# Kernel tuning notes

Measured on AMD Instinct MI355X. Metric: run time of the kernel, lower is better.

The kernel has to match this reference:

```python
import jax, jax.numpy as jnp
import numpy as np


def setup_inputs() -> dict:
    key = jax.random.key(0)
    k1, k2, k3 = jax.random.split(key, 3)
    B, DIM, H, Wd = 32, 512, 64, 64
    K, DQ = 64, 3
    features = jax.random.normal(k1, (B, DIM, H, Wd), dtype=jnp.float32)
    query = jax.random.normal(k2, (B, DQ, H, Wd), dtype=jnp.float32)
    # Ensemble of K 1x1 convs (no bias): weight [K, dim_query, dim], scaled like conv init
    W = jax.random.normal(k3, (K, DQ, DIM), dtype=jnp.float32) * (1.0 / np.sqrt(DIM))
    return {"features": features, "query": query, "W": W}


def reference(features, query, W):
    B = query.shape[0]
    # ensemble 1x1 conv: key_values [k, b, q, h, w]
    kv = jnp.einsum('kqd,bdhw->kbqhw', W, features)
    # rearrange 'k b ... -> b k ...'
    kv_b = jnp.transpose(kv, (1, 0, 2, 3, 4))          # [b, k, q, h, w]
    q_flat = query.reshape(B, 1, -1)                    # [b, 1, N]
    kv_flat = kv_b.reshape(B, kv_b.shape[1], -1)        # [b, k, N]
    # torch.cdist (p=2) between [b,1,N] and [b,k,N] -> [b,k]
    diff = q_flat - kv_flat
    distance = jnp.sqrt(jnp.sum(diff * diff, axis=-1))  # [b, k]
    codes = jnp.argmin(distance, axis=-1)               # [b]
    # batched gather of selected key_values
    idx = codes[:, None, None, None, None]
    sel_key_values = jnp.take_along_axis(kv_b, idx, axis=1)[:, 0]  # [b, q, h, w]
    commit_loss = jnp.mean((sel_key_values - query) ** 2)
    return sel_key_values, codes, commit_loss
```

## Files before the change

kernel.cpp:

```cpp
#include <hip/hip_runtime.h>
#include <hip/hip_bf16.h>
#include <hip/hip_fp16.h>

#define BN   32
#define DIMK 512
#define HW   4096
#define KK   64
#define DQ   3
#define RR   192
#define NT   128
#define NBLK (HW / NT)

typedef _Float16 half8  __attribute__((ext_vector_type(8)));
typedef float    f32x4  __attribute__((ext_vector_type(4)));
typedef short    short8 __attribute__((ext_vector_type(8)));

#define A16_OFF    0
#define A16_BYTES  (RR * DIMK * 2)
#define DIST2_OFF  196608
#define DIST2_BYTES (BN * KK * 4)
#define KV_OFF     262144
#define KV_BYTES   ((size_t)BN * RR * HW * 2)

#define OUT_SEL    ((size_t)BN * DQ * HW)
#define OUT_LOSS   (OUT_SEL + BN)

__global__ void init_kernel(const float* __restrict__ Wsrc,
                            _Float16* __restrict__ A16,
                            float* __restrict__ dist2,
                            float* __restrict__ out) {
  int gid = blockIdx.x * 256 + threadIdx.x;
  if (gid < RR * DIMK) A16[gid] = (_Float16)Wsrc[gid];
  if (gid < BN * KK)   dist2[gid] = 0.f;
  if (gid == 0)        out[OUT_LOSS] = 0.f;
}

template <bool STORE>
__global__ __launch_bounds__(256) void gemm_dist_kernel(
    const float* __restrict__ f, const float* __restrict__ query,
    const _Float16* __restrict__ A16, __hip_bfloat16* __restrict__ kv,
    float* __restrict__ dist2) {
  __shared__ __align__(16) _Float16 Alds[2][RR][40];
  __shared__ __align__(16) _Float16 Blds[2][4][NT][8];
  __shared__ float qlds[DQ][NT];
  __shared__ float rowsum[RR];

  const int t  = threadIdx.x;
  const int w  = t >> 6;
  const int l  = t & 63;
  const int lq = l >> 4;
  const int ln = l & 15;
  const int b  = blockIdx.y;
  const int n0 = blockIdx.x * NT;

  for (int s = t; s < DQ * NT; s += 256) {
    int q = s / NT, n = s % NT;
    qlds[q][n] = query[((size_t)b * DQ + q) * HW + n0 + n];
  }

  f32x4 acc[3][8];
#pragma unroll
  for (int mt = 0; mt < 3; mt++)
#pragma unroll
    for (int nt = 0; nt < 8; nt++) acc[mt][nt] = (f32x4)0.f;

  const int bn  = t & (NT - 1);
  const int bkb = t >> 7;

  float bpre[16];
  half8 apre[3];

  auto loadTile = [&](int kk) {
    const float* fp = f + ((size_t)b * DIMK + kk * 32 + bkb * 16) * HW + n0 + bn;
#pragma unroll
    for (int j = 0; j < 16; j++) bpre[j] = fp[(size_t)j * HW];
#pragma unroll
    for (int i = 0; i < 3; i++) {
      int s = t + i * 256;
      int m = s >> 2, oct = s & 3;
      apre[i] = *(const half8*)&A16[m * DIMK + kk * 32 + oct * 8];
    }
  };
  auto stageTile = [&](int buf) {
#pragma unroll
    for (int i = 0; i < 3; i++) {
      int s = t + i * 256;
      int m = s >> 2, oct = s & 3;
      *(half8*)&Alds[buf][m][oct * 8] = apre[i];
    }
    half8 h0, h1;
#pragma unroll
    for (int j = 0; j < 8; j++) { h0[j] = (_Float16)bpre[j]; h1[j] = (_Float16)bpre[8 + j]; }
    *(half8*)&Blds[buf][2 * bkb][bn][0]     = h0;
    *(half8*)&Blds[buf][2 * bkb + 1][bn][0] = h1;
  };

  loadTile(0);
  stageTile(0);
  for (int kk = 0; kk < DIMK / 32; kk++) {
    const int cur = kk & 1;
    __syncthreads();
    if (kk < DIMK / 32 - 1) loadTile(kk + 1);

    half8 af[3], bf[8];
#pragma unroll
    for (int mt = 0; mt < 3; mt++)
      af[mt] = *(const half8*)&Alds[cur][w * 48 + mt * 16 + ln][lq * 8];
#pragma unroll
    for (int nt = 0; nt < 8; nt++)
      bf[nt] = *(const half8*)&Blds[cur][lq][nt * 16 + ln][0];
#pragma unroll
    for (int mt = 0; mt < 3; mt++)
#pragma unroll
      for (int nt = 0; nt < 8; nt++)
        acc[mt][nt] = __builtin_amdgcn_mfma_f32_16x16x32_f16(af[mt], bf[nt],
                                                             acc[mt][nt], 0, 0, 0);
    if (kk < DIMK / 32 - 1) stageTile(cur ^ 1);
  }

  float rs[3][4];
#pragma unroll
  for (int mt = 0; mt < 3; mt++)
#pragma unroll
    for (int i = 0; i < 4; i++) rs[mt][i] = 0.f;

#pragma unroll
  for (int mt = 0; mt < 3; mt++) {
#pragma unroll
    for (int i = 0; i < 4; i++) {
      int r = w * 48 + mt * 16 + lq * 4 + i;
      int q = r % 3;
#pragma unroll
      for (int nt = 0; nt < 8; nt++) {
        int n = nt * 16 + ln;
        float c = acc[mt][nt][i];
        if (STORE) kv[((size_t)b * RR + r) * HW + n0 + n] = __float2bfloat16(c);
        float d = c - qlds[q][n];
        rs[mt][i] += d * d;
      }
    }
  }
#pragma unroll
  for (int mt = 0; mt < 3; mt++)
#pragma unroll
    for (int i = 0; i < 4; i++) {
      float v = rs[mt][i];
      v += __shfl_xor(v, 1, 64);
      v += __shfl_xor(v, 2, 64);
      v += __shfl_xor(v, 4, 64);
      v += __shfl_xor(v, 8, 64);
      rs[mt][i] = v;
    }
  if (ln < 12) {
    int mt = ln >> 2, i = ln & 3;
    rowsum[w * 48 + mt * 16 + lq * 4 + i] = rs[mt][i];
  }
  __syncthreads();
  if (t < KK) {
    float v = rowsum[3 * t] + rowsum[3 * t + 1] + rowsum[3 * t + 2];
    atomicAdd(&dist2[b * KK + t], v);
  }
}

__global__ __launch_bounds__(256) void gather_kernel(
    const __hip_bfloat16* __restrict__ kv, const float* __restrict__ query,
    const float* __restrict__ dist2, float* __restrict__ out) {
  int b = blockIdx.x, t = threadIdx.x;
  __shared__ int scode;
  __shared__ float red[4];
  if (t == 0) {
    float best = dist2[b * KK]; int bi = 0;
    for (int k = 1; k < KK; k++) {
      float v = dist2[b * KK + k];
      if (v < best) { best = v; bi = k; }
    }
    scode = bi;
    out[OUT_SEL + b] = (float)bi;
  }
  __syncthreads();
  int code = scode;
  const short8* src = (const short8*)(kv + ((size_t)b * RR + code * DQ) * HW);
  const f32x4*  qp  = (const f32x4*)(query + (size_t)b * DQ * HW);
  f32x4*        op  = (f32x4*)(out + (size_t)b * DQ * HW);
  float lsum = 0.f;
  for (int c = t; c < DQ * HW / 8; c += 256) {
    short8 v = src[c];
    f32x4 o0, o1;
#pragma unroll
    for (int j = 0; j < 4; j++) {
      unsigned u0 = ((unsigned)(unsigned short)v[j]) << 16;
      unsigned u1 = ((unsigned)(unsigned short)v[4 + j]) << 16;
      o0[j] = __builtin_bit_cast(float, u0);
      o1[j] = __builtin_bit_cast(float, u1);
    }
    f32x4 q0 = qp[2 * c], q1 = qp[2 * c + 1];
    op[2 * c] = o0; op[2 * c + 1] = o1;
#pragma unroll
    for (int j = 0; j < 4; j++) {
      float d0 = o0[j] - q0[j], d1 = o1[j] - q1[j];
      lsum += d0 * d0 + d1 * d1;
    }
  }
  for (int off = 1; off < 64; off <<= 1) lsum += __shfl_xor(lsum, off, 64);
  if ((t & 63) == 0) red[t >> 6] = lsum;
  __syncthreads();
  if (t == 0)
    atomicAdd(&out[OUT_LOSS],
              (red[0] + red[1] + red[2] + red[3]) * (1.f / (float)(BN * DQ * HW)));
}

__global__ __launch_bounds__(256) void recompute_kernel(
    const float* __restrict__ f, const float* __restrict__ query,
    const float* __restrict__ Wsrc, const float* __restrict__ dist2,
    float* __restrict__ out) {
  int b = blockIdx.y, t = threadIdx.x;
  int hw = blockIdx.x * 256 + t;
  __shared__ int scode;
  __shared__ float red[4];
  if (t == 0) {
    float best = dist2[b * KK]; int bi = 0;
    for (int k = 1; k < KK; k++) {
      float v = dist2[b * KK + k];
      if (v < best) { best = v; bi = k; }
    }
    scode = bi;
    if (blockIdx.x == 0) out[OUT_SEL + b] = (float)bi;
  }
  __syncthreads();
  int code = scode;
  const float* w0 = Wsrc + (size_t)code * DQ * DIMK;
  const float* fp = f + (size_t)b * DIMK * HW + hw;
  float a0 = 0.f, a1 = 0.f, a2 = 0.f;
  for (int d = 0; d < DIMK; d++) {
    float fv = fp[(size_t)d * HW];
    a0 += w0[d] * fv;
    a1 += w0[DIMK + d] * fv;
    a2 += w0[2 * DIMK + d] * fv;
  }
  const float* qp = query + (size_t)b * DQ * HW;
  float* op = out + (size_t)b * DQ * HW;
  op[hw] = a0; op[HW + hw] = a1; op[2 * HW + hw] = a2;
  float d0 = a0 - qp[hw], d1 = a1 - qp[HW + hw], d2 = a2 - qp[2 * HW + hw];
  float lsum = d0 * d0 + d1 * d1 + d2 * d2;
  for (int off = 1; off < 64; off <<= 1) lsum += __shfl_xor(lsum, off, 64);
  if ((t & 63) == 0) red[t >> 6] = lsum;
  __syncthreads();
  if (t == 0)
    atomicAdd(&out[OUT_LOSS],
              (red[0] + red[1] + red[2] + red[3]) * (1.f / (float)(BN * DQ * HW)));
}

extern "C" void kernel_launch(void* const* d_in, const int* in_sizes, int n_in,
                              void* d_out, int out_size, void* d_ws, size_t ws_size,
                              hipStream_t stream) {
  const float* f     = (const float*)d_in[0];
  const float* query = (const float*)d_in[1];
  const float* Wsrc  = (const float*)d_in[2];
  float* out = (float*)d_out;
  char*  ws  = (char*)d_ws;

  _Float16*        A16   = (_Float16*)(ws + A16_OFF);
  float*           dist2 = (float*)(ws + DIST2_OFF);
  __hip_bfloat16*  kv    = (__hip_bfloat16*)(ws + KV_OFF);

  const bool store = ws_size >= (size_t)KV_OFF + KV_BYTES;

  init_kernel<<<384, 256, 0, stream>>>(Wsrc, A16, dist2, out);
  if (store) {
    gemm_dist_kernel<true><<<dim3(NBLK, BN), 256, 0, stream>>>(f, query, A16, kv, dist2);
    gather_kernel<<<BN, 256, 0, stream>>>(kv, query, dist2, out);
  } else {
    gemm_dist_kernel<false><<<dim3(NBLK, BN), 256, 0, stream>>>(f, query, A16, nullptr, dist2);
    recompute_kernel<<<dim3(HW / 256, BN), 256, 0, stream>>>(f, query, Wsrc, dist2, out);
  }
}
```

Before: 380.5 us.

## Load A fragments directly from global, vectorize B loads, replace atomics with partials

Drops the LDS staging of the weight matrix: each wave reads its A fragments straight from global (L2-resident fp16 weights) into registers, prefetched one k-step ahead. The feature tile is now loaded with float2 vector loads, and the MFMA loop is split into two halves to shorten register live ranges. Per-block distance atomics are replaced by a deterministic partial-sum buffer that the gather kernel reduces, which also removes the zeroing in the init kernel. The cost is extra global traffic for A, since each wave re-reads its rows, and a serial 32-element reduction per code in the gather kernel.

```diff
diff --git a/kernel.cpp b/kernel.cpp
--- a/kernel.cpp
+++ b/kernel.cpp
@@ -12,14 +12,15 @@
 #define NBLK (HW / NT)
 
 typedef _Float16 half8  __attribute__((ext_vector_type(8)));
+typedef float    f32x2  __attribute__((ext_vector_type(2)));
 typedef float    f32x4  __attribute__((ext_vector_type(4)));
 typedef short    short8 __attribute__((ext_vector_type(8)));
 
 #define A16_OFF    0
 #define A16_BYTES  (RR * DIMK * 2)
-#define DIST2_OFF  196608
-#define DIST2_BYTES (BN * KK * 4)
-#define KV_OFF     262144
+#define PART_OFF   196608
+#define PART_BYTES (BN * NBLK * KK * 4)
+#define KV_OFF     524288
 #define KV_BYTES   ((size_t)BN * RR * HW * 2)
 
 #define OUT_SEL    ((size_t)BN * DQ * HW)
@@ -27,11 +28,9 @@
 
 __global__ void init_kernel(const float* __restrict__ Wsrc,
                             _Float16* __restrict__ A16,
-                            float* __restrict__ dist2,
                             float* __restrict__ out) {
   int gid = blockIdx.x * 256 + threadIdx.x;
   if (gid < RR * DIMK) A16[gid] = (_Float16)Wsrc[gid];
-  if (gid < BN * KK)   dist2[gid] = 0.f;
   if (gid == 0)        out[OUT_LOSS] = 0.f;
 }
 
@@ -39,8 +38,7 @@
 __global__ __launch_bounds__(256) void gemm_dist_kernel(
     const float* __restrict__ f, const float* __restrict__ query,
     const _Float16* __restrict__ A16, __hip_bfloat16* __restrict__ kv,
-    float* __restrict__ dist2) {
-  __shared__ __align__(16) _Float16 Alds[2][RR][40];
+    float* __restrict__ partial) {
   __shared__ __align__(16) _Float16 Blds[2][4][NT][8];
   __shared__ float qlds[DQ][NT];
   __shared__ float rowsum[RR];
@@ -64,58 +62,62 @@
 #pragma unroll
     for (int nt = 0; nt < 8; nt++) acc[mt][nt] = (f32x4)0.f;
 
-  const int bn  = t & (NT - 1);
-  const int bkb = t >> 7;
-
-  float bpre[16];
+  const int bn  = t & 63;
+  const int bkb = t >> 6;
+
+  f32x2 bpre[8];
   half8 apre[3];
 
-  auto loadTile = [&](int kk) {
-    const float* fp = f + ((size_t)b * DIMK + kk * 32 + bkb * 16) * HW + n0 + bn;
-#pragma unroll
-    for (int j = 0; j < 16; j++) bpre[j] = fp[(size_t)j * HW];
-#pragma unroll
-    for (int i = 0; i < 3; i++) {
-      int s = t + i * 256;
-      int m = s >> 2, oct = s & 3;
-      apre[i] = *(const half8*)&A16[m * DIMK + kk * 32 + oct * 8];
-    }
+  const int arow = w * 48 + ln;
+
+  auto loadB = [&](int kk) {
+    const float* fp = f + ((size_t)b * DIMK + kk * 32 + bkb * 8) * HW + n0 + 2 * bn;
+#pragma unroll
+    for (int j = 0; j < 8; j++) bpre[j] = *(const f32x2*)&fp[(size_t)j * HW];
   };
-  auto stageTile = [&](int buf) {
-#pragma unroll
-    for (int i = 0; i < 3; i++) {
-      int s = t + i * 256;
-      int m = s >> 2, oct = s & 3;
-      *(half8*)&Alds[buf][m][oct * 8] = apre[i];
-    }
+  auto loadA = [&](int kk) {
+#pragma unroll
+    for (int mt = 0; mt < 3; mt++)
+      apre[mt] = *(const half8*)&A16[(arow + mt * 16) * DIMK + kk * 32 + lq * 8];
+  };
+  auto stageB = [&](int buf) {
     half8 h0, h1;
 #pragma unroll
-    for (int j = 0; j < 8; j++) { h0[j] = (_Float16)bpre[j]; h1[j] = (_Float16)bpre[8 + j]; }
-    *(half8*)&Blds[buf][2 * bkb][bn][0]     = h0;
-    *(half8*)&Blds[buf][2 * bkb + 1][bn][0] = h1;
+    for (int j = 0; j < 8; j++) {
+      h0[j] = (_Float16)bpre[j][0];
+      h1[j] = (_Float16)bpre[j][1];
+    }
+    *(half8*)&Blds[buf][bkb][2 * bn][0]     = h0;
+    *(half8*)&Blds[buf][bkb][2 * bn + 1][0] = h1;
   };
 
-  loadTile(0);
-  stageTile(0);
+  loadA(0);
+  loadB(0);
+  stageB(0);
   for (int kk = 0; kk < DIMK / 32; kk++) {
     const int cur = kk & 1;
     __syncthreads();
-    if (kk < DIMK / 32 - 1) loadTile(kk + 1);
-
-    half8 af[3], bf[8];
-#pragma unroll
-    for (int mt = 0; mt < 3; mt++)
-      af[mt] = *(const half8*)&Alds[cur][w * 48 + mt * 16 + ln][lq * 8];
-#pragma unroll
-    for (int nt = 0; nt < 8; nt++)
-      bf[nt] = *(const half8*)&Blds[cur][lq][nt * 16 + ln][0];
-#pragma unroll
-    for (int mt = 0; mt < 3; mt++)
-#pragma unroll
-      for (int nt = 0; nt < 8; nt++)
-        acc[mt][nt] = __builtin_amdgcn_mfma_f32_16x16x32_f16(af[mt], bf[nt],
-                                                             acc[mt][nt], 0, 0, 0);
-    if (kk < DIMK / 32 - 1) stageTile(cur ^ 1);
+    if (kk < DIMK / 32 - 1) loadB(kk + 1);
+
+    half8 af[3];
+#pragma unroll
+    for (int mt = 0; mt < 3; mt++) af[mt] = apre[mt];
+    if (kk < DIMK / 32 - 1) loadA(kk + 1);
+
+#pragma unroll
+    for (int h = 0; h < 2; h++) {
+      half8 bf[4];
+#pragma unroll
+      for (int n4 = 0; n4 < 4; n4++)
+        bf[n4] = *(const half8*)&Blds[cur][lq][h * 64 + n4 * 16 + ln][0];
+#pragma unroll
+      for (int mt = 0; mt < 3; mt++)
+#pragma unroll
+        for (int n4 = 0; n4 < 4; n4++)
+          acc[mt][h * 4 + n4] = __builtin_amdgcn_mfma_f32_16x16x32_f16(
+              af[mt], bf[n4], acc[mt][h * 4 + n4], 0, 0, 0);
+    }
+    if (kk < DIMK / 32 - 1) stageB(cur ^ 1);
   }
 
   float rs[3][4];
@@ -156,24 +158,28 @@
     rowsum[w * 48 + mt * 16 + lq * 4 + i] = rs[mt][i];
   }
   __syncthreads();
-  if (t < KK) {
-    float v = rowsum[3 * t] + rowsum[3 * t + 1] + rowsum[3 * t + 2];
-    atomicAdd(&dist2[b * KK + t], v);
-  }
+  if (t < KK)
+    partial[((size_t)b * NBLK + blockIdx.x) * KK + t] =
+        rowsum[3 * t] + rowsum[3 * t + 1] + rowsum[3 * t + 2];
 }
 
 __global__ __launch_bounds__(256) void gather_kernel(
     const __hip_bfloat16* __restrict__ kv, const float* __restrict__ query,
-    const float* __restrict__ dist2, float* __restrict__ out) {
+    const float* __restrict__ partial, float* __restrict__ out) {
   int b = blockIdx.x, t = threadIdx.x;
+  __shared__ float dsum[KK];
   __shared__ int scode;
   __shared__ float red[4];
+  if (t < KK) {
+    float s = 0.f;
+    for (int x = 0; x < NBLK; x++) s += partial[((size_t)b * NBLK + x) * KK + t];
+    dsum[t] = s;
+  }
+  __syncthreads();
   if (t == 0) {
-    float best = dist2[b * KK]; int bi = 0;
-    for (int k = 1; k < KK; k++) {
-      float v = dist2[b * KK + k];
-      if (v < best) { best = v; bi = k; }
-    }
+    float best = dsum[0]; int bi = 0;
+    for (int k = 1; k < KK; k++)
+      if (dsum[k] < best) { best = dsum[k]; bi = k; }
     scode = bi;
     out[OUT_SEL + b] = (float)bi;
   }
@@ -211,18 +217,23 @@
 
 __global__ __launch_bounds__(256) void recompute_kernel(
     const float* __restrict__ f, const float* __restrict__ query,
-    const float* __restrict__ Wsrc, const float* __restrict__ dist2,
+    const float* __restrict__ Wsrc, const float* __restrict__ partial,
     float* __restrict__ out) {
   int b = blockIdx.y, t = threadIdx.x;
   int hw = blockIdx.x * 256 + t;
+  __shared__ float dsum[KK];
   __shared__ int scode;
   __shared__ float red[4];
+  if (t < KK) {
+    float s = 0.f;
+    for (int x = 0; x < NBLK; x++) s += partial[((size_t)b * NBLK + x) * KK + t];
+    dsum[t] = s;
+  }
+  __syncthreads();
   if (t == 0) {
-    float best = dist2[b * KK]; int bi = 0;
-    for (int k = 1; k < KK; k++) {
-      float v = dist2[b * KK + k];
-      if (v < best) { best = v; bi = k; }
-    }
+    float best = dsum[0]; int bi = 0;
+    for (int k = 1; k < KK; k++)
+      if (dsum[k] < best) { best = dsum[k]; bi = k; }
     scode = bi;
     if (blockIdx.x == 0) out[OUT_SEL + b] = (float)bi;
   }
@@ -259,18 +270,18 @@
   float* out = (float*)d_out;
   char*  ws  = (char*)d_ws;
 
-  _Float16*        A16   = (_Float16*)(ws + A16_OFF);
-  float*           dist2 = (float*)(ws + DIST2_OFF);
-  __hip_bfloat16*  kv    = (__hip_bfloat16*)(ws + KV_OFF);
+  _Float16*        A16     = (_Float16*)(ws + A16_OFF);
+  float*           partial = (float*)(ws + PART_OFF);
+  __hip_bfloat16*  kv      = (__hip_bfloat16*)(ws + KV_OFF);
 
   const bool store = ws_size >= (size_t)KV_OFF + KV_BYTES;
 
-  init_kernel<<<384, 256, 0, stream>>>(Wsrc, A16, dist2, out);
+  init_kernel<<<384, 256, 0, stream>>>(Wsrc, A16, out);
   if (store) {
-    gemm_dist_kernel<true><<<dim3(NBLK, BN), 256, 0, stream>>>(f, query, A16, kv, dist2);
-    gather_kernel<<<BN, 256, 0, stream>>>(kv, query, dist2, out);
+    gemm_dist_kernel<true><<<dim3(NBLK, BN), 256, 0, stream>>>(f, query, A16, kv, partial);
+    gather_kernel<<<BN, 256, 0, stream>>>(kv, query, partial, out);
   } else {
-    gemm_dist_kernel<false><<<dim3(NBLK, BN), 256, 0, stream>>>(f, query, A16, nullptr, dist2);
-    recompute_kernel<<<dim3(HW / 256, BN), 256, 0, stream>>>(f, query, Wsrc, dist2, out);
-  }
-}
+    gemm_dist_kernel<false><<<dim3(NBLK, BN), 256, 0, stream>>>(f, query, A16, nullptr, partial);
+    recompute_kernel<<<dim3(HW / 256, BN), 256, 0, stream>>>(f, query, Wsrc, partial, out);
+  }
+}
```

Result: slower. 390.2 us (+2.5%).
